# Kernel tuning notes

Hardware: AMD Instinct MI355X
Metric: run time of the kernel (lower is better)

The kernel has to match this reference:

```python
import jax, jax.numpy as jnp
import numpy as np

CAUSAL = True

def setup_inputs() -> dict:
    key = jax.random.key(0)
    kq, kk, kv = jax.random.split(key, 3)
    B, S, H, D = 2, 2048, 16, 64
    q = jax.random.normal(kq, (B, S, H, D), dtype=jnp.float32)
    k = jax.random.normal(kk, (B, S, H, D), dtype=jnp.float32)
    v = jax.random.normal(kv, (B, S, H, D), dtype=jnp.float32)
    return {"q": q, "k": k, "v": v}

def reference(q, k, v):
    # q,k,v: [B, S, H, D]
    B, Sq, H, D = q.shape
    Sk = k.shape[1]
    scale = 1.0 / jnp.sqrt(jnp.asarray(D, dtype=q.dtype))
    # scores: [B, H, Sq, Sk]
    scores = jnp.einsum('bqhd,bkhd->bhqk', q * scale, k)
    if CAUSAL:
        causal_mask = jnp.triu(jnp.ones((Sq, Sk), dtype=bool), k=1)
        scores = jnp.where(causal_mask, -jnp.inf, scores)
    attn = jax.nn.softmax(scores, axis=-1)
    # output: [B, Sq, H, D]
    out = jnp.einsum('bhqk,bkhd->bqhd', attn, v)
    return out
```

## Files before the change

### kernel.cpp

```cpp
#include <hip/hip_runtime.h>


typedef __bf16  bf16x8_t  __attribute__((ext_vector_type(8)));
typedef short   short4_t  __attribute__((ext_vector_type(4)));
typedef float   f32x4     __attribute__((ext_vector_type(4)));

#define MFMA_K32(a, b, c) __builtin_amdgcn_mfma_f32_16x16x32_bf16((a), (b), (c), 0, 0, 0)

__device__ __forceinline__ f32x4 mfma_k16(short4_t a, short4_t b, f32x4 c) {
#if defined(__HIP_DEVICE_COMPILE__)
    return __builtin_amdgcn_mfma_f32_16x16x16bf16_1k(a, b, c, 0, 0, 0);
#else
    return c;
#endif
}

constexpr int   SEQ = 2048, NH = 16;
constexpr int   SROW = NH * 64;
constexpr float QS   = 0.125f * 1.44269504088896f;

__device__ __forceinline__ unsigned f2bfu(float f) {
    unsigned u = __builtin_bit_cast(unsigned, f);
    return (u + 0x7fffu + ((u >> 16) & 1u)) >> 16;
}
__device__ __forceinline__ unsigned pk2(float x, float y) {
#if defined(__HIP_DEVICE_COMPILE__) && __has_builtin(__builtin_amdgcn_cvt_pk_bf16_f32)
    typedef __bf16 bfv2 __attribute__((ext_vector_type(2)));
    bfv2 v = __builtin_amdgcn_cvt_pk_bf16_f32(x, y);
    return __builtin_bit_cast(unsigned, v);
#else
    return (f2bfu(x) & 0xffffu) | (f2bfu(y) << 16);
#endif
}

__global__ __launch_bounds__(128, 2) void fa_fwd(const float* __restrict__ Q,
                                                 const float* __restrict__ K,
                                                 const float* __restrict__ V,
                                                 float* __restrict__ O) {
    const int id = blockIdx.x;
    const int bh = id & 31;
    const int g  = id >> 5;
    const int b  = bh >> 4, h = bh & 15;
    const int T  = (g < 16) ? (31 - g) : (g - 16);
    const int nkt = T + 1;

    const int tid  = threadIdx.x;
    const int wave = tid >> 6;
    const int lane = tid & 63;
    const int lhi  = lane >> 4;
    const int llo  = lane & 15;
    const int q0   = T * 64 + wave * 32;

    __shared__ __align__(16) unsigned short Kl[64][72];
    __shared__ __align__(16) unsigned short Vt[64][72];

    bf16x8_t qf[2][2];
#pragma unroll
    for (int mt = 0; mt < 2; ++mt)
#pragma unroll
        for (int ks = 0; ks < 2; ++ks) {
            const float* qp = Q + (size_t)((b * SEQ + q0 + mt * 16 + llo) * SROW + h * 64 + ks * 32 + lhi * 8);
            float4 a = ((const float4*)qp)[0], c = ((const float4*)qp)[1];
            uint4 u;
            u.x = pk2(a.x * QS, a.y * QS); u.y = pk2(a.z * QS, a.w * QS);
            u.z = pk2(c.x * QS, c.y * QS); u.w = pk2(c.z * QS, c.w * QS);
            qf[mt][ks] = __builtin_bit_cast(bf16x8_t, u);
        }

    const float* Kb = K + (size_t)(b * SEQ) * SROW + h * 64;
    const float* Vb = V + (size_t)(b * SEQ) * SROW + h * 64;

    const int skr = tid >> 4;
    const int skc = tid & 15;
    const int va  = tid & 31;
    const int vc  = tid >> 5;
    const int vR  = ((2 * va) >> 3) & 7;
    const int vc0 = (16 * vc + 8 * vR) & 63;
    const int vc1 = (16 * vc + 8 + 8 * vR) & 63;

    float4 pkf[8];
    float2 pvf[16];
#pragma unroll
    for (int p = 0; p < 8; ++p)
        pkf[p] = *(const float4*)(Kb + (size_t)(skr + 8 * p) * SROW + skc * 4);
#pragma unroll
    for (int j = 0; j < 16; ++j)
        pvf[j] = *(const float2*)(Vb + (size_t)(16 * vc + j) * SROW + 2 * va);

    f32x4 acc[2][4], accL[2];
#pragma unroll
    for (int mt = 0; mt < 2; ++mt) {
        accL[mt] = (f32x4){0.f, 0.f, 0.f, 0.f};
#pragma unroll
        for (int dt = 0; dt < 4; ++dt) acc[mt][dt] = (f32x4){0.f, 0.f, 0.f, 0.f};
    }

    short4_t ones;
#pragma unroll
    for (int j = 0; j < 4; ++j) ones[j] = (short)0x3F80;

    for (int kt = 0; kt < nkt; ++kt) {
        const int kv0 = kt * 64;
        __syncthreads();

#pragma unroll
        for (int p = 0; p < 8; ++p)
            *(uint2*)&Kl[skr + 8 * p][skc * 4] =
                make_uint2(pk2(pkf[p].x, pkf[p].y), pk2(pkf[p].z, pkf[p].w));

        {
            uint4 u0a, u0b, u1a, u1b;
            u0a.x = pk2(pvf[0].x,  pvf[1].x);  u0a.y = pk2(pvf[2].x,  pvf[3].x);
            u0a.z = pk2(pvf[4].x,  pvf[5].x);  u0a.w = pk2(pvf[6].x,  pvf[7].x);
            u0b.x = pk2(pvf[8].x,  pvf[9].x);  u0b.y = pk2(pvf[10].x, pvf[11].x);
            u0b.z = pk2(pvf[12].x, pvf[13].x); u0b.w = pk2(pvf[14].x, pvf[15].x);
            u1a.x = pk2(pvf[0].y,  pvf[1].y);  u1a.y = pk2(pvf[2].y,  pvf[3].y);
            u1a.z = pk2(pvf[4].y,  pvf[5].y);  u1a.w = pk2(pvf[6].y,  pvf[7].y);
            u1b.x = pk2(pvf[8].y,  pvf[9].y);  u1b.y = pk2(pvf[10].y, pvf[11].y);
            u1b.z = pk2(pvf[12].y, pvf[13].y); u1b.w = pk2(pvf[14].y, pvf[15].y);
            *(uint4*)&Vt[2 * va    ][vc0] = u0a;
            *(uint4*)&Vt[2 * va    ][vc1] = u0b;
            *(uint4*)&Vt[2 * va + 1][vc0] = u1a;
            *(uint4*)&Vt[2 * va + 1][vc1] = u1b;
        }
        __syncthreads();

        if (kt + 1 < nkt) {
            const float* kb = Kb + (size_t)(kv0 + 64) * SROW;
            const float* vb = Vb + (size_t)(kv0 + 64) * SROW;
#pragma unroll
            for (int p = 0; p < 8; ++p)
                pkf[p] = *(const float4*)(kb + (size_t)(skr + 8 * p) * SROW + skc * 4);
#pragma unroll
            for (int j = 0; j < 16; ++j)
                pvf[j] = *(const float2*)(vb + (size_t)(16 * vc + j) * SROW + 2 * va);
        }

        f32x4 s[2][4];
#pragma unroll
        for (int nt = 0; nt < 4; ++nt) {
            bf16x8_t kf0 = *(const bf16x8_t*)&Kl[nt * 16 + llo][lhi * 8];
            bf16x8_t kf1 = *(const bf16x8_t*)&Kl[nt * 16 + llo][32 + lhi * 8];
#pragma unroll
            for (int mt = 0; mt < 2; ++mt) {
                f32x4 z = (f32x4){0.f, 0.f, 0.f, 0.f};
                z = MFMA_K32(kf0, qf[mt][0], z);
                z = MFMA_K32(kf1, qf[mt][1], z);
                s[mt][nt] = z;
            }
        }

#pragma unroll
        for (int mt = 0; mt < 2; ++mt) {
            if (kv0 + 63 > q0 + mt * 16) {
                const int m_g = q0 + mt * 16 + llo;
#pragma unroll
                for (int nt = 0; nt < 4; ++nt)
#pragma unroll
                    for (int r = 0; r < 4; ++r)
                        if (kv0 + nt * 16 + lhi * 4 + r > m_g) s[mt][nt][r] = -INFINITY;
            }
        }

        short4_t pf[2][4];
#pragma unroll
        for (int mt = 0; mt < 2; ++mt)
#pragma unroll
            for (int nt = 0; nt < 4; ++nt) {
                uint2 u = make_uint2(
                    pk2(__builtin_amdgcn_exp2f(s[mt][nt][0]), __builtin_amdgcn_exp2f(s[mt][nt][1])),
                    pk2(__builtin_amdgcn_exp2f(s[mt][nt][2]), __builtin_amdgcn_exp2f(s[mt][nt][3])));
                pf[mt][nt] = __builtin_bit_cast(short4_t, u);
            }

#pragma unroll
        for (int ks = 0; ks < 4; ++ks) {
#pragma unroll
            for (int dt = 0; dt < 4; ++dt) {
                const int d   = dt * 16 + llo;
                const int col = (ks * 16 + lhi * 4 + 8 * ((d >> 3) & 7)) & 63;
                uint2 vu = *(const uint2*)&Vt[d][col];
                short4_t vf = __builtin_bit_cast(short4_t, vu);
#pragma unroll
                for (int mt = 0; mt < 2; ++mt)
                    acc[mt][dt] = mfma_k16(pf[mt][ks], vf, acc[mt][dt]);
            }
#pragma unroll
            for (int mt = 0; mt < 2; ++mt)
                accL[mt] = mfma_k16(pf[mt][ks], ones, accL[mt]);
        }
    }

#pragma unroll
    for (int mt = 0; mt < 2; ++mt)
#pragma unroll
        for (int r = 0; r < 4; ++r) {
            const float inv = 1.0f / accL[mt][r];
            float* ob = O + (size_t)((b * SEQ + q0 + mt * 16 + lhi * 4 + r) * SROW + h * 64);
#pragma unroll
            for (int dt = 0; dt < 4; ++dt) ob[dt * 16 + llo] = acc[mt][dt][r] * inv;
        }
}

extern "C" void kernel_launch(void* const* d_in, const int* in_sizes, int n_in,
                              void* d_out, int out_size, void* d_ws, size_t ws_size,
                              hipStream_t stream) {
    const float* q = (const float*)d_in[0];
    const float* k = (const float*)d_in[1];
    const float* v = (const float*)d_in[2];
    float* o = (float*)d_out;
    fa_fwd<<<dim3(1024), dim3(128), 0, stream>>>(q, k, v, o);
}
```

Baseline: 149.3 us.

## Pair causal query tiles per block with four waves of sixteen rows each

```diff
diff --git a/kernel.cpp b/kernel.cpp
--- a/kernel.cpp
+++ b/kernel.cpp
@@ -33,173 +33,172 @@
 #endif
 }
 
-__global__ __launch_bounds__(128, 2) void fa_fwd(const float* __restrict__ Q,
+__global__ __launch_bounds__(256, 2) void fa_fwd(const float* __restrict__ Q,
                                                  const float* __restrict__ K,
                                                  const float* __restrict__ V,
                                                  float* __restrict__ O) {
     const int id = blockIdx.x;
     const int bh = id & 31;
-    const int g  = id >> 5;
+    const int pr = id >> 5;
     const int b  = bh >> 4, h = bh & 15;
-    const int T  = (g < 16) ? (31 - g) : (g - 16);
-    const int nkt = T + 1;
+    const int T0 = 31 - pr;
+    const int T1 = pr;
 
     const int tid  = threadIdx.x;
     const int wave = tid >> 6;
     const int lane = tid & 63;
     const int lhi  = lane >> 4;
     const int llo  = lane & 15;
-    const int q0   = T * 64 + wave * 32;
 
     __shared__ __align__(16) unsigned short Kl[64][72];
     __shared__ __align__(16) unsigned short Vt[64][72];
 
     bf16x8_t qf[2][2];
 #pragma unroll
-    for (int mt = 0; mt < 2; ++mt)
+    for (int ph = 0; ph < 2; ++ph) {
+        const int Tq = ph ? T1 : T0;
 #pragma unroll
         for (int ks = 0; ks < 2; ++ks) {
-            const float* qp = Q + (size_t)((b * SEQ + q0 + mt * 16 + llo) * SROW + h * 64 + ks * 32 + lhi * 8);
+            const float* qp = Q + (size_t)((b * SEQ + Tq * 64 + wave * 16 + llo) * SROW + h * 64 + ks * 32 + lhi * 8);
             float4 a = ((const float4*)qp)[0], c = ((const float4*)qp)[1];
             uint4 u;
             u.x = pk2(a.x * QS, a.y * QS); u.y = pk2(a.z * QS, a.w * QS);
             u.z = pk2(c.x * QS, c.y * QS); u.w = pk2(c.z * QS, c.w * QS);
-            qf[mt][ks] = __builtin_bit_cast(bf16x8_t, u);
-        }
+            qf[ph][ks] = __builtin_bit_cast(bf16x8_t, u);
+        }
+    }
 
     const float* Kb = K + (size_t)(b * SEQ) * SROW + h * 64;
     const float* Vb = V + (size_t)(b * SEQ) * SROW + h * 64;
 
     const int skr = tid >> 4;
     const int skc = tid & 15;
-    const int va  = tid & 31;
-    const int vc  = tid >> 5;
-    const int vR  = ((2 * va) >> 3) & 7;
-    const int vc0 = (16 * vc + 8 * vR) & 63;
-    const int vc1 = (16 * vc + 8 + 8 * vR) & 63;
-
-    float4 pkf[8];
-    float2 pvf[16];
-#pragma unroll
-    for (int p = 0; p < 8; ++p)
-        pkf[p] = *(const float4*)(Kb + (size_t)(skr + 8 * p) * SROW + skc * 4);
-#pragma unroll
-    for (int j = 0; j < 16; ++j)
-        pvf[j] = *(const float2*)(Vb + (size_t)(16 * vc + j) * SROW + 2 * va);
-
-    f32x4 acc[2][4], accL[2];
-#pragma unroll
-    for (int mt = 0; mt < 2; ++mt) {
-        accL[mt] = (f32x4){0.f, 0.f, 0.f, 0.f};
-#pragma unroll
-        for (int dt = 0; dt < 4; ++dt) acc[mt][dt] = (f32x4){0.f, 0.f, 0.f, 0.f};
-    }
+    const int va   = tid & 31;
+    const int vc   = tid >> 5;
+    const int vcol = (8 * vc + 8 * (va >> 2)) & 63;
+
+    float4 pkf[4];
+    float2 pvf[8];
+#pragma unroll
+    for (int p = 0; p < 4; ++p)
+        pkf[p] = *(const float4*)(Kb + (size_t)(skr + 16 * p) * SROW + skc * 4);
+#pragma unroll
+    for (int j = 0; j < 8; ++j)
+        pvf[j] = *(const float2*)(Vb + (size_t)(8 * vc + j) * SROW + 2 * va);
+
+    f32x4 acc[4], accL;
+    accL = (f32x4){0.f, 0.f, 0.f, 0.f};
+#pragma unroll
+    for (int dt = 0; dt < 4; ++dt) acc[dt] = (f32x4){0.f, 0.f, 0.f, 0.f};
 
     short4_t ones;
 #pragma unroll
     for (int j = 0; j < 4; ++j) ones[j] = (short)0x3F80;
 
-    for (int kt = 0; kt < nkt; ++kt) {
+    const int split = T0 + 1;
+
+    for (int it = 0; it < 33; ++it) {
+        const int ph = (it >= split);
+
+        if (it == split) {
+            const int q0e = T0 * 64 + wave * 16;
+#pragma unroll
+            for (int r = 0; r < 4; ++r) {
+                const float inv = 1.0f / accL[r];
+                float* ob = O + (size_t)((b * SEQ + q0e + lhi * 4 + r) * SROW + h * 64);
+#pragma unroll
+                for (int dt = 0; dt < 4; ++dt) ob[dt * 16 + llo] = acc[dt][r] * inv;
+            }
+            accL = (f32x4){0.f, 0.f, 0.f, 0.f};
+#pragma unroll
+            for (int dt = 0; dt < 4; ++dt) acc[dt] = (f32x4){0.f, 0.f, 0.f, 0.f};
+        }
+
+        const int kt  = ph ? it - split : it;
+        const int q0  = (ph ? T1 : T0) * 64 + wave * 16;
         const int kv0 = kt * 64;
+
         __syncthreads();
 
 #pragma unroll
-        for (int p = 0; p < 8; ++p)
-            *(uint2*)&Kl[skr + 8 * p][skc * 4] =
+        for (int p = 0; p < 4; ++p)
+            *(uint2*)&Kl[skr + 16 * p][skc * 4] =
                 make_uint2(pk2(pkf[p].x, pkf[p].y), pk2(pkf[p].z, pkf[p].w));
 
         {
-            uint4 u0a, u0b, u1a, u1b;
-            u0a.x = pk2(pvf[0].x,  pvf[1].x);  u0a.y = pk2(pvf[2].x,  pvf[3].x);
-            u0a.z = pk2(pvf[4].x,  pvf[5].x);  u0a.w = pk2(pvf[6].x,  pvf[7].x);
-            u0b.x = pk2(pvf[8].x,  pvf[9].x);  u0b.y = pk2(pvf[10].x, pvf[11].x);
-            u0b.z = pk2(pvf[12].x, pvf[13].x); u0b.w = pk2(pvf[14].x, pvf[15].x);
-            u1a.x = pk2(pvf[0].y,  pvf[1].y);  u1a.y = pk2(pvf[2].y,  pvf[3].y);
-            u1a.z = pk2(pvf[4].y,  pvf[5].y);  u1a.w = pk2(pvf[6].y,  pvf[7].y);
-            u1b.x = pk2(pvf[8].y,  pvf[9].y);  u1b.y = pk2(pvf[10].y, pvf[11].y);
-            u1b.z = pk2(pvf[12].y, pvf[13].y); u1b.w = pk2(pvf[14].y, pvf[15].y);
-            *(uint4*)&Vt[2 * va    ][vc0] = u0a;
-            *(uint4*)&Vt[2 * va    ][vc1] = u0b;
-            *(uint4*)&Vt[2 * va + 1][vc0] = u1a;
-            *(uint4*)&Vt[2 * va + 1][vc1] = u1b;
+            uint4 u0, u1;
+            u0.x = pk2(pvf[0].x, pvf[1].x); u0.y = pk2(pvf[2].x, pvf[3].x);
+            u0.z = pk2(pvf[4].x, pvf[5].x); u0.w = pk2(pvf[6].x, pvf[7].x);
+            u1.x = pk2(pvf[0].y, pvf[1].y); u1.y = pk2(pvf[2].y, pvf[3].y);
+            u1.z = pk2(pvf[4].y, pvf[5].y); u1.w = pk2(pvf[6].y, pvf[7].y);
+            *(uint4*)&Vt[2 * va    ][vcol] = u0;
+            *(uint4*)&Vt[2 * va + 1][vcol] = u1;
         }
         __syncthreads();
 
-        if (kt + 1 < nkt) {
-            const float* kb = Kb + (size_t)(kv0 + 64) * SROW;
-            const float* vb = Vb + (size_t)(kv0 + 64) * SROW;
-#pragma unroll
-            for (int p = 0; p < 8; ++p)
-                pkf[p] = *(const float4*)(kb + (size_t)(skr + 8 * p) * SROW + skc * 4);
-#pragma unroll
-            for (int j = 0; j < 16; ++j)
-                pvf[j] = *(const float2*)(vb + (size_t)(16 * vc + j) * SROW + 2 * va);
-        }
-
-        f32x4 s[2][4];
+        if (it + 1 < 33) {
+            const int kt2 = (it + 1 >= split) ? (it + 1 - split) : (it + 1);
+            const float* kb = Kb + (size_t)(kt2 * 64) * SROW;
+            const float* vb = Vb + (size_t)(kt2 * 64) * SROW;
+#pragma unroll
+            for (int p = 0; p < 4; ++p)
+                pkf[p] = *(const float4*)(kb + (size_t)(skr + 16 * p) * SROW + skc * 4);
+#pragma unroll
+            for (int j = 0; j < 8; ++j)
+                pvf[j] = *(const float2*)(vb + (size_t)(8 * vc + j) * SROW + 2 * va);
+        }
+
+        f32x4 s[4];
 #pragma unroll
         for (int nt = 0; nt < 4; ++nt) {
             bf16x8_t kf0 = *(const bf16x8_t*)&Kl[nt * 16 + llo][lhi * 8];
             bf16x8_t kf1 = *(const bf16x8_t*)&Kl[nt * 16 + llo][32 + lhi * 8];
-#pragma unroll
-            for (int mt = 0; mt < 2; ++mt) {
-                f32x4 z = (f32x4){0.f, 0.f, 0.f, 0.f};
-                z = MFMA_K32(kf0, qf[mt][0], z);
-                z = MFMA_K32(kf1, qf[mt][1], z);
-                s[mt][nt] = z;
-            }
-        }
-
-#pragma unroll
-        for (int mt = 0; mt < 2; ++mt) {
-            if (kv0 + 63 > q0 + mt * 16) {
-                const int m_g = q0 + mt * 16 + llo;
-#pragma unroll
-                for (int nt = 0; nt < 4; ++nt)
-#pragma unroll
-                    for (int r = 0; r < 4; ++r)
-                        if (kv0 + nt * 16 + lhi * 4 + r > m_g) s[mt][nt][r] = -INFINITY;
-            }
-        }
-
-        short4_t pf[2][4];
-#pragma unroll
-        for (int mt = 0; mt < 2; ++mt)
-#pragma unroll
-            for (int nt = 0; nt < 4; ++nt) {
-                uint2 u = make_uint2(
-                    pk2(__builtin_amdgcn_exp2f(s[mt][nt][0]), __builtin_amdgcn_exp2f(s[mt][nt][1])),
-                    pk2(__builtin_amdgcn_exp2f(s[mt][nt][2]), __builtin_amdgcn_exp2f(s[mt][nt][3])));
-                pf[mt][nt] = __builtin_bit_cast(short4_t, u);
-            }
+            f32x4 z = (f32x4){0.f, 0.f, 0.f, 0.f};
+            z = MFMA_K32(kf0, qf[ph][0], z);
+            z = MFMA_K32(kf1, qf[ph][1], z);
+            s[nt] = z;
+        }
+
+        if (kv0 + 63 > q0) {
+            const int m_g = q0 + llo;
+#pragma unroll
+            for (int nt = 0; nt < 4; ++nt)
+#pragma unroll
+                for (int r = 0; r < 4; ++r)
+                    if (kv0 + nt * 16 + lhi * 4 + r > m_g) s[nt][r] = -INFINITY;
+        }
+
+        short4_t pf[4];
+#pragma unroll
+        for (int nt = 0; nt < 4; ++nt) {
+            uint2 u = make_uint2(
+                pk2(__builtin_amdgcn_exp2f(s[nt][0]), __builtin_amdgcn_exp2f(s[nt][1])),
+                pk2(__builtin_amdgcn_exp2f(s[nt][2]), __builtin_amdgcn_exp2f(s[nt][3])));
+            pf[nt] = __builtin_bit_cast(short4_t, u);
+        }
 
 #pragma unroll
         for (int ks = 0; ks < 4; ++ks) {
 #pragma unroll
             for (int dt = 0; dt < 4; ++dt) {
                 const int d   = dt * 16 + llo;
-                const int col = (ks * 16 + lhi * 4 + 8 * ((d >> 3) & 7)) & 63;
+                const int col = (ks * 16 + lhi * 4 + 8 * (d >> 3)) & 63;
                 uint2 vu = *(const uint2*)&Vt[d][col];
                 short4_t vf = __builtin_bit_cast(short4_t, vu);
-#pragma unroll
-                for (int mt = 0; mt < 2; ++mt)
-                    acc[mt][dt] = mfma_k16(pf[mt][ks], vf, acc[mt][dt]);
+                acc[dt] = mfma_k16(pf[ks], vf, acc[dt]);
             }
-#pragma unroll
-            for (int mt = 0; mt < 2; ++mt)
-                accL[mt] = mfma_k16(pf[mt][ks], ones, accL[mt]);
+            accL = mfma_k16(pf[ks], ones, accL);
         }
     }
 
-#pragma unroll
-    for (int mt = 0; mt < 2; ++mt)
-#pragma unroll
-        for (int r = 0; r < 4; ++r) {
-            const float inv = 1.0f / accL[mt][r];
-            float* ob = O + (size_t)((b * SEQ + q0 + mt * 16 + lhi * 4 + r) * SROW + h * 64);
-#pragma unroll
-            for (int dt = 0; dt < 4; ++dt) ob[dt * 16 + llo] = acc[mt][dt][r] * inv;
-        }
+    const int q0e = T1 * 64 + wave * 16;
+#pragma unroll
+    for (int r = 0; r < 4; ++r) {
+        const float inv = 1.0f / accL[r];
+        float* ob = O + (size_t)((b * SEQ + q0e + lhi * 4 + r) * SROW + h * 64);
+#pragma unroll
+        for (int dt = 0; dt < 4; ++dt) ob[dt * 16 + llo] = acc[dt][r] * inv;
+    }
 }
 
 extern "C" void kernel_launch(void* const* d_in, const int* in_sizes, int n_in,
@@ -209,5 +208,5 @@
     const float* k = (const float*)d_in[1];
     const float* v = (const float*)d_in[2];
     float* o = (float*)d_out;
-    fa_fwd<<<dim3(1024), dim3(128), 0, stream>>>(q, k, v, o);
-}
+    fa_fwd<<<dim3(512), dim3(256), 0, stream>>>(q, k, v, o);
+}
```

Measured after the change: 130.7 us. -12.4%, faster.

## Prepack K/V into bf16 MFMA fragments and split keys across waves

Applied to the files above, without the earlier changes.

```diff
diff --git a/kernel.cpp b/kernel.cpp
--- a/kernel.cpp
+++ b/kernel.cpp
@@ -33,173 +33,196 @@
 #endif
 }
 
-__global__ __launch_bounds__(128, 2) void fa_fwd(const float* __restrict__ Q,
-                                                 const float* __restrict__ K,
-                                                 const float* __restrict__ V,
+__global__ __launch_bounds__(256) void prepack(const float* __restrict__ K,
+                                               const float* __restrict__ V,
+                                               unsigned short* __restrict__ Kp,
+                                               unsigned short* __restrict__ Vp) {
+    const int blk = blockIdx.x;
+    const int tid = threadIdx.x;
+    if (blk < 1024) {
+        const int bh = blk >> 5, c = blk & 31;
+        const int b  = bh >> 4,  h = bh & 15;
+        const int nt = tid >> 6, lane = tid & 63;
+        const int llo = lane & 15, lhi = lane >> 4;
+        const float* src = K + (size_t)(b * SEQ + c * 64 + nt * 16 + llo) * SROW + h * 64;
+#pragma unroll
+        for (int ks = 0; ks < 2; ++ks) {
+            const float4* p = (const float4*)(src + ks * 32 + lhi * 8);
+            float4 a = p[0], d4 = p[1];
+            uint4 u;
+            u.x = pk2(a.x, a.y);   u.y = pk2(a.z, a.w);
+            u.z = pk2(d4.x, d4.y); u.w = pk2(d4.z, d4.w);
+            *(uint4*)(Kp + (size_t)(bh * 32 + c) * 4096 + (nt * 2 + ks) * 512 + lane * 8) = u;
+        }
+    } else {
+        const int q  = blk - 1024;
+        const int bh = q >> 5, c = q & 31;
+        const int b  = bh >> 4, h = bh & 15;
+        const int dt = tid >> 6, lane = tid & 63;
+        const int llo = lane & 15, lhi = lane >> 4;
+        const float* src = V + (size_t)(b * SEQ + c * 64 + lhi * 4) * SROW + h * 64 + dt * 16 + llo;
+#pragma unroll
+        for (int kq = 0; kq < 4; ++kq) {
+            const float* s2 = src + (size_t)(kq * 16) * SROW;
+            float f0 = s2[0], f1 = s2[SROW], f2 = s2[2 * SROW], f3 = s2[3 * SROW];
+            uint2 u;
+            u.x = pk2(f0, f1); u.y = pk2(f2, f3);
+            *(uint2*)(Vp + (size_t)(bh * 32 + c) * 4096 + (kq * 4 + dt) * 256 + lane * 4) = u;
+        }
+    }
+}
+
+__global__ __launch_bounds__(256, 4) void fa_fwd(const float* __restrict__ Q,
+                                                 const unsigned short* __restrict__ Kp,
+                                                 const unsigned short* __restrict__ Vp,
                                                  float* __restrict__ O) {
     const int id = blockIdx.x;
     const int bh = id & 31;
-    const int g  = id >> 5;
+    const int pr = id >> 5;
     const int b  = bh >> 4, h = bh & 15;
-    const int T  = (g < 16) ? (31 - g) : (g - 16);
-    const int nkt = T + 1;
+    const int T0 = 63 - pr;
+    const int T1 = pr;
+    const int split = (T0 >> 1) + 1;
 
     const int tid  = threadIdx.x;
-    const int wave = tid >> 6;
+    const int w    = tid >> 6;
     const int lane = tid & 63;
     const int lhi  = lane >> 4;
     const int llo  = lane & 15;
-    const int q0   = T * 64 + wave * 32;
-
-    __shared__ __align__(16) unsigned short Kl[64][72];
-    __shared__ __align__(16) unsigned short Vt[64][72];
+
+    __shared__ __align__(16) float Red[4][5][64][4];
+
+    const unsigned short* Kbh = Kp + (size_t)bh * (32 * 4096);
+    const unsigned short* Vbh = Vp + (size_t)bh * (32 * 4096);
+
+    const int koff0 = (w * 2 + 0) * 512 + lane * 8;
+    const int koff1 = (w * 2 + 1) * 512 + lane * 8;
+    const int voff  = (w * 4) * 256 + lane * 4;
 
     bf16x8_t qf[2][2];
-#pragma unroll
-    for (int mt = 0; mt < 2; ++mt)
-#pragma unroll
-        for (int ks = 0; ks < 2; ++ks) {
-            const float* qp = Q + (size_t)((b * SEQ + q0 + mt * 16 + llo) * SROW + h * 64 + ks * 32 + lhi * 8);
-            float4 a = ((const float4*)qp)[0], c = ((const float4*)qp)[1];
-            uint4 u;
-            u.x = pk2(a.x * QS, a.y * QS); u.y = pk2(a.z * QS, a.w * QS);
-            u.z = pk2(c.x * QS, c.y * QS); u.w = pk2(c.z * QS, c.w * QS);
-            qf[mt][ks] = __builtin_bit_cast(bf16x8_t, u);
-        }
-
-    const float* Kb = K + (size_t)(b * SEQ) * SROW + h * 64;
-    const float* Vb = V + (size_t)(b * SEQ) * SROW + h * 64;
-
-    const int skr = tid >> 4;
-    const int skc = tid & 15;
-    const int va  = tid & 31;
-    const int vc  = tid >> 5;
-    const int vR  = ((2 * va) >> 3) & 7;
-    const int vc0 = (16 * vc + 8 * vR) & 63;
-    const int vc1 = (16 * vc + 8 + 8 * vR) & 63;
-
-    float4 pkf[8];
-    float2 pvf[16];
-#pragma unroll
-    for (int p = 0; p < 8; ++p)
-        pkf[p] = *(const float4*)(Kb + (size_t)(skr + 8 * p) * SROW + skc * 4);
-#pragma unroll
-    for (int j = 0; j < 16; ++j)
-        pvf[j] = *(const float2*)(Vb + (size_t)(16 * vc + j) * SROW + 2 * va);
+    auto loadQ = [&](int Tq) {
+#pragma unroll
+        for (int mt = 0; mt < 2; ++mt)
+#pragma unroll
+            for (int ks = 0; ks < 2; ++ks) {
+                const float* qp = Q + (size_t)(b * SEQ + Tq * 32 + mt * 16 + llo) * SROW + h * 64 + ks * 32 + lhi * 8;
+                float4 a = ((const float4*)qp)[0], c4 = ((const float4*)qp)[1];
+                uint4 u;
+                u.x = pk2(a.x * QS, a.y * QS); u.y = pk2(a.z * QS, a.w * QS);
+                u.z = pk2(c4.x * QS, c4.y * QS); u.w = pk2(c4.z * QS, c4.w * QS);
+                qf[mt][ks] = __builtin_bit_cast(bf16x8_t, u);
+            }
+    };
 
     f32x4 acc[2][4], accL[2];
-#pragma unroll
-    for (int mt = 0; mt < 2; ++mt) {
-        accL[mt] = (f32x4){0.f, 0.f, 0.f, 0.f};
-#pragma unroll
-        for (int dt = 0; dt < 4; ++dt) acc[mt][dt] = (f32x4){0.f, 0.f, 0.f, 0.f};
+    auto clearAcc = [&]() {
+#pragma unroll
+        for (int mt = 0; mt < 2; ++mt) {
+            accL[mt] = (f32x4){0.f, 0.f, 0.f, 0.f};
+#pragma unroll
+            for (int dt = 0; dt < 4; ++dt) acc[mt][dt] = (f32x4){0.f, 0.f, 0.f, 0.f};
+        }
+    };
+
+    auto finish = [&](int Tq) {
+        const int q0 = Tq * 32;
+#pragma unroll
+        for (int mt = 0; mt < 2; ++mt) {
+#pragma unroll
+            for (int dt = 0; dt < 4; ++dt) *(f32x4*)&Red[w][dt][lane][0] = acc[mt][dt];
+            *(f32x4*)&Red[w][4][lane][0] = accL[mt];
+            __syncthreads();
+            f32x4 oc = (f32x4){0.f, 0.f, 0.f, 0.f};
+            f32x4 ls = (f32x4){0.f, 0.f, 0.f, 0.f};
+#pragma unroll
+            for (int u = 0; u < 4; ++u) {
+                oc += *(const f32x4*)&Red[u][w][lane][0];
+                ls += *(const f32x4*)&Red[u][4][lane][0];
+            }
+#pragma unroll
+            for (int r = 0; r < 4; ++r)
+                O[(size_t)(b * SEQ + q0 + mt * 16 + lhi * 4 + r) * SROW + h * 64 + w * 16 + llo] = oc[r] / ls[r];
+            __syncthreads();
+        }
+    };
+
+    loadQ(T0);
+    clearAcc();
+
+    short4_t ones;
+#pragma unroll
+    for (int j = 0; j < 4; ++j) ones[j] = (short)0x3F80;
+
+    uint4 kc0 = *(const uint4*)(Kbh + koff0);
+    uint4 kc1 = *(const uint4*)(Kbh + koff1);
+
+    for (int it = 0; it < 33; ++it) {
+        const int ph = (it >= split);
+
+        if (it == split) {
+            finish(T0);
+            clearAcc();
+            loadQ(T1);
+        }
+
+        const int kt  = ph ? it - split : it;
+        const int q0  = (ph ? T1 : T0) * 32;
+        const int kv0 = kt * 64;
+        const size_t cb = (size_t)kt * 4096;
+
+        uint4 kn0, kn1;
+        const bool more = (it + 1 < 33);
+        if (more) {
+            const int ktn = (it + 1 >= split) ? (it + 1 - split) : (it + 1);
+            kn0 = *(const uint4*)(Kbh + (size_t)ktn * 4096 + koff0);
+            kn1 = *(const uint4*)(Kbh + (size_t)ktn * 4096 + koff1);
+        }
+        uint2 vc[4];
+#pragma unroll
+        for (int dt = 0; dt < 4; ++dt)
+            vc[dt] = *(const uint2*)(Vbh + cb + voff + dt * 256);
+
+        f32x4 s[2];
+#pragma unroll
+        for (int mt = 0; mt < 2; ++mt) {
+            f32x4 z = (f32x4){0.f, 0.f, 0.f, 0.f};
+            z = MFMA_K32(__builtin_bit_cast(bf16x8_t, kc0), qf[mt][0], z);
+            z = MFMA_K32(__builtin_bit_cast(bf16x8_t, kc1), qf[mt][1], z);
+            s[mt] = z;
+        }
+
+#pragma unroll
+        for (int mt = 0; mt < 2; ++mt) {
+            if (kv0 + w * 16 + 15 > q0 + mt * 16) {
+                const int m_g = q0 + mt * 16 + llo;
+#pragma unroll
+                for (int r = 0; r < 4; ++r)
+                    if (kv0 + w * 16 + lhi * 4 + r > m_g) s[mt][r] = -INFINITY;
+            }
+        }
+
+        short4_t pf[2];
+#pragma unroll
+        for (int mt = 0; mt < 2; ++mt) {
+            uint2 u = make_uint2(
+                pk2(__builtin_amdgcn_exp2f(s[mt][0]), __builtin_amdgcn_exp2f(s[mt][1])),
+                pk2(__builtin_amdgcn_exp2f(s[mt][2]), __builtin_amdgcn_exp2f(s[mt][3])));
+            pf[mt] = __builtin_bit_cast(short4_t, u);
+        }
+
+#pragma unroll
+        for (int dt = 0; dt < 4; ++dt) {
+            short4_t vf = __builtin_bit_cast(short4_t, vc[dt]);
+            acc[0][dt] = mfma_k16(pf[0], vf, acc[0][dt]);
+            acc[1][dt] = mfma_k16(pf[1], vf, acc[1][dt]);
+        }
+        accL[0] = mfma_k16(pf[0], ones, accL[0]);
+        accL[1] = mfma_k16(pf[1], ones, accL[1]);
+
+        if (more) { kc0 = kn0; kc1 = kn1; }
     }
 
-    short4_t ones;
-#pragma unroll
-    for (int j = 0; j < 4; ++j) ones[j] = (short)0x3F80;
-
-    for (int kt = 0; kt < nkt; ++kt) {
-        const int kv0 = kt * 64;
-        __syncthreads();
-
-#pragma unroll
-        for (int p = 0; p < 8; ++p)
-            *(uint2*)&Kl[skr + 8 * p][skc * 4] =
-                make_uint2(pk2(pkf[p].x, pkf[p].y), pk2(pkf[p].z, pkf[p].w));
-
-        {
-            uint4 u0a, u0b, u1a, u1b;
-            u0a.x = pk2(pvf[0].x,  pvf[1].x);  u0a.y = pk2(pvf[2].x,  pvf[3].x);
-            u0a.z = pk2(pvf[4].x,  pvf[5].x);  u0a.w = pk2(pvf[6].x,  pvf[7].x);
-            u0b.x = pk2(pvf[8].x,  pvf[9].x);  u0b.y = pk2(pvf[10].x, pvf[11].x);
-            u0b.z = pk2(pvf[12].x, pvf[13].x); u0b.w = pk2(pvf[14].x, pvf[15].x);
-            u1a.x = pk2(pvf[0].y,  pvf[1].y);  u1a.y = pk2(pvf[2].y,  pvf[3].y);
-            u1a.z = pk2(pvf[4].y,  pvf[5].y);  u1a.w = pk2(pvf[6].y,  pvf[7].y);
-            u1b.x = pk2(pvf[8].y,  pvf[9].y);  u1b.y = pk2(pvf[10].y, pvf[11].y);
-            u1b.z = pk2(pvf[12].y, pvf[13].y); u1b.w = pk2(pvf[14].y, pvf[15].y);
-            *(uint4*)&Vt[2 * va    ][vc0] = u0a;
-            *(uint4*)&Vt[2 * va    ][vc1] = u0b;
-            *(uint4*)&Vt[2 * va + 1][vc0] = u1a;
-            *(uint4*)&Vt[2 * va + 1][vc1] = u1b;
-        }
-        __syncthreads();
-
-        if (kt + 1 < nkt) {
-            const float* kb = Kb + (size_t)(kv0 + 64) * SROW;
-            const float* vb = Vb + (size_t)(kv0 + 64) * SROW;
-#pragma unroll
-            for (int p = 0; p < 8; ++p)
-                pkf[p] = *(const float4*)(kb + (size_t)(skr + 8 * p) * SROW + skc * 4);
-#pragma unroll
-            for (int j = 0; j < 16; ++j)
-                pvf[j] = *(const float2*)(vb + (size_t)(16 * vc + j) * SROW + 2 * va);
-        }
-
-        f32x4 s[2][4];
-#pragma unroll
-        for (int nt = 0; nt < 4; ++nt) {
-            bf16x8_t kf0 = *(const bf16x8_t*)&Kl[nt * 16 + llo][lhi * 8];
-            bf16x8_t kf1 = *(const bf16x8_t*)&Kl[nt * 16 + llo][32 + lhi * 8];
-#pragma unroll
-            for (int mt = 0; mt < 2; ++mt) {
-                f32x4 z = (f32x4){0.f, 0.f, 0.f, 0.f};
-                z = MFMA_K32(kf0, qf[mt][0], z);
-                z = MFMA_K32(kf1, qf[mt][1], z);
-                s[mt][nt] = z;
-            }
-        }
-
-#pragma unroll
-        for (int mt = 0; mt < 2; ++mt) {
-            if (kv0 + 63 > q0 + mt * 16) {
-                const int m_g = q0 + mt * 16 + llo;
-#pragma unroll
-                for (int nt = 0; nt < 4; ++nt)
-#pragma unroll
-                    for (int r = 0; r < 4; ++r)
-                        if (kv0 + nt * 16 + lhi * 4 + r > m_g) s[mt][nt][r] = -INFINITY;
-            }
-        }
-
-        short4_t pf[2][4];
-#pragma unroll
-        for (int mt = 0; mt < 2; ++mt)
-#pragma unroll
-            for (int nt = 0; nt < 4; ++nt) {
-                uint2 u = make_uint2(
-                    pk2(__builtin_amdgcn_exp2f(s[mt][nt][0]), __builtin_amdgcn_exp2f(s[mt][nt][1])),
-                    pk2(__builtin_amdgcn_exp2f(s[mt][nt][2]), __builtin_amdgcn_exp2f(s[mt][nt][3])));
-                pf[mt][nt] = __builtin_bit_cast(short4_t, u);
-            }
-
-#pragma unroll
-        for (int ks = 0; ks < 4; ++ks) {
-#pragma unroll
-            for (int dt = 0; dt < 4; ++dt) {
-                const int d   = dt * 16 + llo;
-                const int col = (ks * 16 + lhi * 4 + 8 * ((d >> 3) & 7)) & 63;
-                uint2 vu = *(const uint2*)&Vt[d][col];
-                short4_t vf = __builtin_bit_cast(short4_t, vu);
-#pragma unroll
-                for (int mt = 0; mt < 2; ++mt)
-                    acc[mt][dt] = mfma_k16(pf[mt][ks], vf, acc[mt][dt]);
-            }
-#pragma unroll
-            for (int mt = 0; mt < 2; ++mt)
-                accL[mt] = mfma_k16(pf[mt][ks], ones, accL[mt]);
-        }
-    }
-
-#pragma unroll
-    for (int mt = 0; mt < 2; ++mt)
-#pragma unroll
-        for (int r = 0; r < 4; ++r) {
-            const float inv = 1.0f / accL[mt][r];
-            float* ob = O + (size_t)((b * SEQ + q0 + mt * 16 + lhi * 4 + r) * SROW + h * 64);
-#pragma unroll
-            for (int dt = 0; dt < 4; ++dt) ob[dt * 16 + llo] = acc[mt][dt][r] * inv;
-        }
+    finish(T1);
 }
 
 extern "C" void kernel_launch(void* const* d_in, const int* in_sizes, int n_in,
@@ -209,5 +232,8 @@
     const float* k = (const float*)d_in[1];
     const float* v = (const float*)d_in[2];
     float* o = (float*)d_out;
-    fa_fwd<<<dim3(1024), dim3(128), 0, stream>>>(q, k, v, o);
-}
+    unsigned short* Kp = (unsigned short*)d_ws;
+    unsigned short* Vp = Kp + (size_t)32 * 32 * 4096;
+    prepack<<<dim3(2048), dim3(256), 0, stream>>>(k, v, Kp, Vp);
+    fa_fwd<<<dim3(1024), dim3(256), 0, stream>>>(q, Kp, Vp, o);
+}
```

New measurement: 126.5 us. 15.3% less time.
